# Kernel optimization log

Hardware: AMD Instinct MI355X
Metric: run time of the kernel (lower is better)

The kernel has to match this reference:

```python
import jax, jax.numpy as jnp
import numpy as np
import math

V, D, H, L, F, S, B = 32000, 1024, 16, 4, 4096, 1024, 2
DK = D // H
EPS = 1e-5


def _pe(seq_len, d_model):
    pos = jnp.arange(seq_len, dtype=jnp.float32)[:, None]
    div = jnp.exp(jnp.arange(0, d_model, 2, dtype=jnp.float32) * (-math.log(10000.0) / d_model))
    ang = pos * div  # [S, D/2]
    return jnp.stack([jnp.sin(ang), jnp.cos(ang)], axis=-1).reshape(seq_len, d_model)


def _ln(x, g, b):
    m = jnp.mean(x, axis=-1, keepdims=True)
    v = jnp.mean(jnp.square(x - m), axis=-1, keepdims=True)
    return (x - m) * jax.lax.rsqrt(v + EPS) * g + b


def setup_inputs() -> dict:
    key = jax.random.key(0)
    ks = jax.random.split(key, 12)
    std = 0.02
    inp = {
        "input_ids": jax.random.randint(ks[0], (B, S), 0, V, dtype=jnp.int32),
        "embed": std * jax.random.normal(ks[1], (V, D), dtype=jnp.float32),
        "Wq": std * jax.random.normal(ks[2], (L, D, D), dtype=jnp.float32),
        "bq": jnp.zeros((L, D), jnp.float32),
        "Wk": std * jax.random.normal(ks[3], (L, D, D), dtype=jnp.float32),
        "bk": jnp.zeros((L, D), jnp.float32),
        "Wv": std * jax.random.normal(ks[4], (L, D, D), dtype=jnp.float32),
        "bv": jnp.zeros((L, D), jnp.float32),
        "Wo": std * jax.random.normal(ks[5], (L, D, D), dtype=jnp.float32),
        "bo": jnp.zeros((L, D), jnp.float32),
        "ln1_g": jnp.ones((L, D), jnp.float32), "ln1_b": jnp.zeros((L, D), jnp.float32),
        "W1": std * jax.random.normal(ks[6], (L, F, D), dtype=jnp.float32),
        "b1": jnp.zeros((L, F), jnp.float32),
        "W2": std * jax.random.normal(ks[7], (L, D, F), dtype=jnp.float32),
        "b2": jnp.zeros((L, D), jnp.float32),
        "ln2_g": jnp.ones((L, D), jnp.float32), "ln2_b": jnp.zeros((L, D), jnp.float32),
        "lnf_g": jnp.ones((D,), jnp.float32), "lnf_b": jnp.zeros((D,), jnp.float32),
        "head_w": std * jax.random.normal(ks[8], (V, D), dtype=jnp.float32),
    }
    return inp


def _forward(input_ids, embed, Wq, bq, Wk, bk, Wv, bv, Wo, bo,
             ln1_g, ln1_b, W1, b1, W2, b2, ln2_g, ln2_b, lnf_g, lnf_b, head_w):
    b, s = input_ids.shape
    x = embed[input_ids] * jnp.float32(math.sqrt(D))  # [B,S,D]
    x = x + _pe(s, D)[None, :, :]
    causal = jnp.tril(jnp.ones((s, s), dtype=bool))  # [S,S]
    scale = jnp.float32(1.0 / math.sqrt(DK))
    for l in range(L):
        q = (x @ Wq[l].T + bq[l]).reshape(b, s, H, DK).transpose(0, 2, 1, 3)
        k = (x @ Wk[l].T + bk[l]).reshape(b, s, H, DK).transpose(0, 2, 1, 3)
        v = (x @ Wv[l].T + bv[l]).reshape(b, s, H, DK).transpose(0, 2, 1, 3)
        scores = jnp.einsum('bhqd,bhkd->bhqk', q, k) * scale
        scores = jnp.where(causal[None, None], scores, jnp.float32(-1e9))
        attn = jax.nn.softmax(scores, axis=-1)
        o = jnp.einsum('bhqk,bhkd->bhqd', attn, v).transpose(0, 2, 1, 3).reshape(b, s, D)
        o = o @ Wo[l].T + bo[l]
        x = _ln(x + o, ln1_g[l], ln1_b[l])
        ff = jax.nn.relu(x @ W1[l].T + b1[l]) @ W2[l].T + b2[l]
        x = _ln(x + ff, ln2_g[l], ln2_b[l])
    x = _ln(x, lnf_g, lnf_b)
    return x @ head_w.T  # logits [B,S,V]


def reference(input_ids, embed, Wq, bq, Wk, bk, Wv, bv, Wo, bo,
              ln1_g, ln1_b, W1, b1, W2, b2, ln2_g, ln2_b, lnf_g, lnf_b, head_w):
    return _forward(input_ids, embed, Wq, bq, Wk, bk, Wv, bv, Wo, bo,
                    ln1_g, ln1_b, W1, b1, W2, b2, ln2_g, ln2_b, lnf_g, lnf_b, head_w)
```

## Files before the change

kernel.cpp:

```cpp
#include <hip/hip_runtime.h>
#include <math.h>


namespace {
constexpr int kV  = 32000;
constexpr int kD  = 1024;
constexpr int kH  = 16;
constexpr int kL  = 4;
constexpr int kF  = 4096;
constexpr int kS  = 1024;
constexpr int kB  = 2;
constexpr int kDK = 64;
constexpr int kM  = kB * kS;
constexpr float kEps   = 1e-5f;
constexpr float kScale = 0.125f;
}

using short8 = __attribute__((ext_vector_type(8))) short;
using f32x4  = __attribute__((ext_vector_type(4))) float;

__device__ __forceinline__ unsigned short f2bf(float f) {
  union { float f; unsigned int u; } x{f};
  const unsigned int r = x.u + 0x7fffu + ((x.u >> 16) & 1u);
  return (unsigned short)(r >> 16);
}

__device__ __forceinline__ void llds16(const void* g, void* l) {
  __builtin_amdgcn_global_load_lds(
      (const __attribute__((address_space(1))) unsigned int*)g,
      (__attribute__((address_space(3))) unsigned int*)l, 16, 0, 0);
}

__device__ __forceinline__ float block_sum256(float v, float* scratch) {
#pragma unroll
  for (int off = 32; off > 0; off >>= 1) v += __shfl_down(v, off, 64);
  const int wid  = threadIdx.x >> 6;
  const int lane = threadIdx.x & 63;
  __syncthreads();
  if (lane == 0) scratch[wid] = v;
  __syncthreads();
  return scratch[0] + scratch[1] + scratch[2] + scratch[3];
}

__global__ __launch_bounds__(256) void f2bf_kernel(const float* __restrict__ in,
                                                   unsigned short* __restrict__ out,
                                                   int n4) {
  const int i = blockIdx.x * 256 + threadIdx.x;
  if (i < n4) {
    const float4 v = ((const float4*)in)[i];
    ushort4 o;
    o.x = f2bf(v.x); o.y = f2bf(v.y); o.z = f2bf(v.z); o.w = f2bf(v.w);
    ((ushort4*)out)[i] = o;
  }
}

__global__ __launch_bounds__(256) void f2bf_layer_kernel(
    const float* __restrict__ wq, const float* __restrict__ wk,
    const float* __restrict__ wv, const float* __restrict__ wo,
    const float* __restrict__ w1, const float* __restrict__ w2,
    unsigned short* __restrict__ dst) {
  const int i = blockIdx.x * 256 + threadIdx.x;
  const float* src;
  size_t so, doff;
  if (i < 1048576) {
    const int seg = i >> 18;
    const int off = i & 262143;
    src = (seg == 0) ? wq : (seg == 1) ? wk : (seg == 2) ? wv : wo;
    so = off;
    doff = (size_t)seg * 1048576 + (size_t)off * 4;
  } else {
    const int j = i - 1048576;
    if (j < 1048576) { src = w1; so = j; doff = 4194304 + (size_t)j * 4; }
    else             { src = w2; so = j - 1048576; doff = 8388608 + (size_t)(j - 1048576) * 4; }
  }
  const float4 v = ((const float4*)src)[so];
  ushort4 o;
  o.x = f2bf(v.x); o.y = f2bf(v.y); o.z = f2bf(v.z); o.w = f2bf(v.w);
  *(ushort4*)(dst + doff) = o;
}

__global__ __launch_bounds__(256) void embed_pe_kernel(
    const int* __restrict__ ids, const float* __restrict__ embed,
    float* __restrict__ x, unsigned short* __restrict__ xb) {
  const int row = blockIdx.x;
  const int s   = row & (kS - 1);
  const int id  = ids[row];
  const float* erow = embed + (size_t)id * kD;
#pragma unroll
  for (int i = 0; i < kD / 256; ++i) {
    const int d = threadIdx.x + i * 256;
    const int p = d >> 1;
    const double div = exp((double)(2 * p) * (-9.210340371976184 / 1024.0));
    const double ang = (double)s * div;
    const float pe = (d & 1) ? (float)cos(ang) : (float)sin(ang);
    const float v = erow[d] * 32.0f + pe;
    x[(size_t)row * kD + d]  = v;
    xb[(size_t)row * kD + d] = f2bf(v);
  }
}

template <int MODE>
__device__ __forceinline__ void gemm_core(int bm, int bn,
                                          const unsigned short* __restrict__ A,
                                          const unsigned short* __restrict__ W,
                                          const float* __restrict__ bias,
                                          void* __restrict__ Cout,
                                          int M, int N, int K,
                                          int k0begin, int k0end, float oscale) {
  __shared__ __align__(16) unsigned short As[128 * 32];
  __shared__ __align__(16) unsigned short Ws[128 * 32];
  const int t    = threadIdx.x;
  const int lane = t & 63;
  const int w    = t >> 6;
  const int wm   = (w >> 1) * 64;
  const int wn   = (w & 1) * 64;
  const int l15  = lane & 15;
  const int quad = lane >> 4;

  f32x4 acc[4][4] = {};

  for (int k0 = k0begin; k0 < k0end; k0 += 32) {
    __syncthreads();
#pragma unroll
    for (int i = 0; i < 2; ++i) {
      const int e   = i * 256 + t;
      const int row = e >> 2;
      const int kc  = (e & 3) * 8;
      const int ldsoff = (i * 256 + w * 64) * 8;
      llds16(A + (size_t)(bm + row) * K + k0 + kc, &As[ldsoff]);
      llds16(W + (size_t)(bn + row) * K + k0 + kc, &Ws[ldsoff]);
    }
    __syncthreads();
    short8 af[4], bf[4];
#pragma unroll
    for (int i = 0; i < 4; ++i)
      af[i] = *(const short8*)&As[(wm + i * 16 + l15) * 32 + quad * 8];
#pragma unroll
    for (int j = 0; j < 4; ++j)
      bf[j] = *(const short8*)&Ws[(wn + j * 16 + l15) * 32 + quad * 8];
#pragma unroll
    for (int i = 0; i < 4; ++i)
#pragma unroll
      for (int j = 0; j < 4; ++j)
        acc[i][j] = __builtin_amdgcn_mfma_f32_16x16x32_bf16(af[i], bf[j], acc[i][j], 0, 0, 0);
  }

#pragma unroll
  for (int i = 0; i < 4; ++i) {
#pragma unroll
    for (int r = 0; r < 4; ++r) {
      const int m = bm + wm + i * 16 + quad * 4 + r;
#pragma unroll
      for (int j = 0; j < 4; ++j) {
        const int n = bn + wn + j * 16 + l15;
        float v = acc[i][j][r] + (bias ? bias[n] : 0.0f);
        if (MODE == 2) v = fmaxf(v, 0.0f);
        if (MODE == 0) {
          ((float*)Cout)[(size_t)m * N + n] = v;
        } else if (MODE == 1) {
          const int b = m >> 10, s = m & 1023;
          const int h = n >> 6,  dk = n & 63;
          ((unsigned short*)Cout)[((size_t)(b * kH + h) * kS + s) * kDK + dk] = f2bf(v * oscale);
        } else if (MODE == 3) {
          const int b = m >> 10, s = m & 1023;
          const int h = n >> 6,  dk = n & 63;
          ((unsigned short*)Cout)[((size_t)(b * kH + h) * kDK + dk) * kS + s] = f2bf(v);
        } else {
          ((unsigned short*)Cout)[(size_t)m * N + n] = f2bf(v);
        }
      }
    }
  }
}

__global__ __launch_bounds__(256) void gemm_head_kernel(
    const unsigned short* __restrict__ A, const unsigned short* __restrict__ W,
    float* __restrict__ C) {
  const int bid = blockIdx.x;
  const int wg  = (bid & 7) * 500 + (bid >> 3);
  const int bm  = (wg & 15) * 128;
  const int bn  = (wg >> 4) * 128;
  gemm_core<0>(bm, bn, A, W, nullptr, C, kM, kV, kD, 0, kD, 1.0f);
}

__global__ __launch_bounds__(256) void gemm_qkv_kernel(
    const unsigned short* __restrict__ A,
    const unsigned short* __restrict__ wq, const unsigned short* __restrict__ wk,
    const unsigned short* __restrict__ wv,
    const float* __restrict__ bq_, const float* __restrict__ bk_,
    const float* __restrict__ bv_,
    unsigned short* __restrict__ qo, unsigned short* __restrict__ ko,
    unsigned short* __restrict__ vo) {
  const int bm = blockIdx.y * 128;
  const int bn = blockIdx.x * 128;
  const int z  = blockIdx.z;
  if (z == 0) {
    gemm_core<1>(bm, bn, A, wq, bq_, qo, kM, kD, kD, 0, kD, kScale);
  } else if (z == 1) {
    gemm_core<1>(bm, bn, A, wk, bk_, ko, kM, kD, kD, 0, kD, 1.0f);
  } else {
    gemm_core<3>(bm, bn, A, wv, bv_, vo, kM, kD, kD, 0, kD, 1.0f);
  }
}

__global__ __launch_bounds__(256) void gemm_splitk_kernel(
    const unsigned short* __restrict__ A, const unsigned short* __restrict__ W,
    const float* __restrict__ bias, float* __restrict__ C0,
    float* __restrict__ C1, int M, int N, int K) {
  const int bm = blockIdx.y * 128;
  const int bn = blockIdx.x * 128;
  if (blockIdx.z == 0)
    gemm_core<0>(bm, bn, A, W, bias, C0, M, N, K, 0, K / 2, 1.0f);
  else
    gemm_core<0>(bm, bn, A, W, nullptr, C1, M, N, K, K / 2, K, 1.0f);
}

__global__ __launch_bounds__(256) void gemm_bf16relu_kernel(
    const unsigned short* __restrict__ A, const unsigned short* __restrict__ W,
    const float* __restrict__ bias, unsigned short* __restrict__ C,
    int M, int N, int K) {
  gemm_core<2>(blockIdx.y * 128, blockIdx.x * 128, A, W, bias, C, M, N, K, 0, K, 1.0f);
}

__global__ __launch_bounds__(256) void attn_mfma_kernel(
    const unsigned short* __restrict__ q, const unsigned short* __restrict__ k,
    const unsigned short* __restrict__ vt, unsigned short* __restrict__ ob) {
  const int bid = blockIdx.x;
  const int wg  = (bid & 7) * 64 + (bid >> 3);
  const int qt  = wg & 15;
  const int h   = (wg >> 4) & 15;
  const int b   = wg >> 8;
  const int q0  = qt * 64;

  __shared__ __align__(16) unsigned short Ks[2][64 * 64];
  __shared__ __align__(16) unsigned short Vs[2][64 * 64];
  __shared__ __align__(16) unsigned short Ps[4][16 * 64];

  const int t    = threadIdx.x;
  const int lane = t & 63;
  const int w    = t >> 6;
  const int l15  = lane & 15;
  const int quad = lane >> 4;

  const size_t base = (size_t)(b * kH + h) * kS * kDK;

  auto stage = [&](int kt_, int buf) {
#pragma unroll
    for (int i = 0; i < 2; ++i) {
      const int e   = i * 256 + t;
      const int row = e >> 3;
      const int g   = e & 7;
      llds16(k + base + (size_t)(kt_ * 64 + row) * kDK + ((g ^ (row & 7)) * 8),
             &Ks[buf][(i * 256 + w * 64) * 8]);
      llds16(vt + base + (size_t)row * kS + kt_ * 64 + ((g ^ (row & 7)) * 8),
             &Vs[buf][(i * 256 + w * 64) * 8]);
    }
  };

  short8 aq[2];
#pragma unroll
  for (int ks = 0; ks < 2; ++ks)
    aq[ks] = *(const short8*)(q + base + (size_t)(q0 + w * 16 + l15) * kDK + ks * 32 + quad * 8);

  f32x4 acc_o[4] = {};
  float m[4]    = {-1e30f, -1e30f, -1e30f, -1e30f};
  float lsum[4] = {0.f, 0.f, 0.f, 0.f};

  stage(0, 0);
  __syncthreads();

  for (int kt = 0; kt <= qt; ++kt) {
    const int cur = kt & 1;
    if (kt < qt) stage(kt + 1, cur ^ 1);

    f32x4 s[4] = {};
#pragma unroll
    for (int j = 0; j < 4; ++j) {
#pragma unroll
      for (int ks = 0; ks < 2; ++ks) {
        const short8 bk8 = *(const short8*)&Ks[cur][(j * 16 + l15) * 64 +
                                                   (((ks * 4 + quad) ^ (l15 & 7)) * 8)];
        s[j] = __builtin_amdgcn_mfma_f32_16x16x32_bf16(aq[ks], bk8, s[j], 0, 0, 0);
      }
    }

    if (kt == qt) {
      const int rb = w * 16 + quad * 4;
#pragma unroll
      for (int j = 0; j < 4; ++j) {
        const int kg = j * 16 + l15;
#pragma unroll
        for (int r = 0; r < 4; ++r)
          if (kg > rb + r) s[j][r] = -1e30f;
      }
    }

    float pm[4];
#pragma unroll
    for (int r = 0; r < 4; ++r)
      pm[r] = fmaxf(fmaxf(s[0][r], s[1][r]), fmaxf(s[2][r], s[3][r]));
#pragma unroll
    for (int off = 8; off > 0; off >>= 1)
#pragma unroll
      for (int r = 0; r < 4; ++r)
        pm[r] = fmaxf(pm[r], __shfl_xor(pm[r], off, 64));

    float alpha[4];
#pragma unroll
    for (int r = 0; r < 4; ++r) {
      const float mn = fmaxf(m[r], pm[r]);
      alpha[r] = __expf(m[r] - mn);
      m[r] = mn;
    }

    float rs[4] = {0.f, 0.f, 0.f, 0.f};
    unsigned short pb16[4][4];
#pragma unroll
    for (int j = 0; j < 4; ++j)
#pragma unroll
      for (int r = 0; r < 4; ++r) {
        const float e = __expf(s[j][r] - m[r]);
        rs[r] += e;
        pb16[j][r] = f2bf(e);
      }
#pragma unroll
    for (int off = 8; off > 0; off >>= 1)
#pragma unroll
      for (int r = 0; r < 4; ++r)
        rs[r] += __shfl_xor(rs[r], off, 64);
#pragma unroll
    for (int r = 0; r < 4; ++r) lsum[r] = lsum[r] * alpha[r] + rs[r];
#pragma unroll
    for (int jd = 0; jd < 4; ++jd)
#pragma unroll
      for (int r = 0; r < 4; ++r) acc_o[jd][r] *= alpha[r];

#pragma unroll
    for (int j = 0; j < 4; ++j)
#pragma unroll
      for (int r = 0; r < 4; ++r) {
        const int row = quad * 4 + r;
        const int col = j * 16 + l15;
        Ps[w][row * 64 + (((col >> 3) ^ (row & 7)) << 3) + (col & 7)] = pb16[j][r];
      }
    asm volatile("s_waitcnt lgkmcnt(0)" ::: "memory");
    __builtin_amdgcn_sched_barrier(0);

    short8 ap[2];
#pragma unroll
    for (int ks = 0; ks < 2; ++ks)
      ap[ks] = *(const short8*)&Ps[w][l15 * 64 + (((ks * 4 + quad) ^ (l15 & 7)) * 8)];

#pragma unroll
    for (int jd = 0; jd < 4; ++jd) {
#pragma unroll
      for (int ks = 0; ks < 2; ++ks) {
        const short8 bv8 = *(const short8*)&Vs[cur][(jd * 16 + l15) * 64 +
                                                   (((ks * 4 + quad) ^ (l15 & 7)) * 8)];
        acc_o[jd] = __builtin_amdgcn_mfma_f32_16x16x32_bf16(ap[ks], bv8, acc_o[jd], 0, 0, 0);
      }
    }

    __syncthreads();
  }

  float inv[4];
#pragma unroll
  for (int r = 0; r < 4; ++r) inv[r] = 1.0f / lsum[r];
#pragma unroll
  for (int jd = 0; jd < 4; ++jd)
#pragma unroll
    for (int r = 0; r < 4; ++r) {
      const int qg = q0 + w * 16 + quad * 4 + r;
      ob[(size_t)(b * kS + qg) * kD + h * kDK + jd * 16 + l15] =
          f2bf(acc_o[jd][r] * inv[r]);
    }
}

__global__ __launch_bounds__(256) void add_ln_kernel(
    float* __restrict__ x, const float* __restrict__ res,
    const float* __restrict__ res2,
    const float* __restrict__ g, const float* __restrict__ bta,
    unsigned short* __restrict__ xb) {
  const int row = blockIdx.x;
  const int t   = threadIdx.x;
  __shared__ float scratch[4];
  float vals[4];
  float sum = 0.f;
  float* xrow = x + (size_t)row * kD;
#pragma unroll
  for (int i = 0; i < 4; ++i) {
    const int d = t + i * 256;
    float vv = xrow[d];
    if (res)  vv += res[(size_t)row * kD + d];
    if (res2) vv += res2[(size_t)row * kD + d];
    vals[i] = vv;
    sum += vv;
  }
  const float mean = block_sum256(sum, scratch) * (1.0f / kD);
  float vsum = 0.f;
#pragma unroll
  for (int i = 0; i < 4; ++i) {
    const float dd = vals[i] - mean;
    vsum += dd * dd;
  }
  const float var  = block_sum256(vsum, scratch) * (1.0f / kD);
  const float rstd = rsqrtf(var + kEps);
#pragma unroll
  for (int i = 0; i < 4; ++i) {
    const int d = t + i * 256;
    const float o = (vals[i] - mean) * rstd * g[d] + bta[d];
    xrow[d] = o;
    xb[(size_t)row * kD + d] = f2bf(o);
  }
}

extern "C" void kernel_launch(void* const* d_in, const int* in_sizes, int n_in,
                              void* d_out, int out_size, void* d_ws, size_t ws_size,
                              hipStream_t stream) {
  const int*   ids   = (const int*)  d_in[0];
  const float* embed = (const float*)d_in[1];
  const float* Wq    = (const float*)d_in[2];
  const float* bq    = (const float*)d_in[3];
  const float* Wk    = (const float*)d_in[4];
  const float* bk    = (const float*)d_in[5];
  const float* Wv    = (const float*)d_in[6];
  const float* bv    = (const float*)d_in[7];
  const float* Wo    = (const float*)d_in[8];
  const float* bo    = (const float*)d_in[9];
  const float* ln1g  = (const float*)d_in[10];
  const float* ln1b  = (const float*)d_in[11];
  const float* W1    = (const float*)d_in[12];
  const float* b1    = (const float*)d_in[13];
  const float* W2    = (const float*)d_in[14];
  const float* b2    = (const float*)d_in[15];
  const float* ln2g  = (const float*)d_in[16];
  const float* ln2b  = (const float*)d_in[17];
  const float* lnfg  = (const float*)d_in[18];
  const float* lnfb  = (const float*)d_in[19];
  const float* headw = (const float*)d_in[20];

  char* ws = (char*)d_ws;
  float*          x    = (float*)          (ws);
  unsigned short* xb   = (unsigned short*) (ws + 8388608);
  unsigned short* qbb  = (unsigned short*) (ws + 12582912);
  unsigned short* kbb  = (unsigned short*) (ws + 16777216);
  unsigned short* vtb  = (unsigned short*) (ws + 20971520);
  unsigned short* ob   = (unsigned short*) (ws + 25165824);
  unsigned short* ff1b = (unsigned short*) (ws + 29360128);
  float*          pb   = (float*)          (ws + 46137344);
  float*          pb2  = (float*)          (ws + 54525952);
  unsigned short* wbuf = (unsigned short*) (ws + 67108864);

  const dim3 blk(256);
  embed_pe_kernel<<<kM, blk, 0, stream>>>(ids, embed, x, xb);

  for (int l = 0; l < kL; ++l) {
    const size_t oD = (size_t)l * kD * kD;
    const size_t oF = (size_t)l * kF * kD;
    f2bf_layer_kernel<<<12288, blk, 0, stream>>>(
        Wq + oD, Wk + oD, Wv + oD, Wo + oD, W1 + oF, W2 + oF, wbuf);

    gemm_qkv_kernel<<<dim3(8, 16, 3), blk, 0, stream>>>(
        xb, wbuf, wbuf + 1048576, wbuf + 2097152,
        bq + (size_t)l * kD, bk + (size_t)l * kD, bv + (size_t)l * kD,
        qbb, kbb, vtb);
    attn_mfma_kernel<<<kB * kH * (kS / 64), blk, 0, stream>>>(qbb, kbb, vtb, ob);
    gemm_splitk_kernel<<<dim3(8, 16, 2), blk, 0, stream>>>(
        ob, wbuf + 3145728, bo + (size_t)l * kD, pb, pb2, kM, kD, kD);
    add_ln_kernel<<<kM, blk, 0, stream>>>(
        x, pb, pb2, ln1g + (size_t)l * kD, ln1b + (size_t)l * kD, xb);
    gemm_bf16relu_kernel<<<dim3(32, 16), blk, 0, stream>>>(
        xb, wbuf + 4194304, b1 + (size_t)l * kF, ff1b, kM, kF, kD);
    gemm_splitk_kernel<<<dim3(8, 16, 2), blk, 0, stream>>>(
        ff1b, wbuf + 8388608, b2 + (size_t)l * kD, pb, pb2, kM, kD, kF);
    add_ln_kernel<<<kM, blk, 0, stream>>>(
        x, pb, pb2, ln2g + (size_t)l * kD, ln2b + (size_t)l * kD, xb);
  }

  add_ln_kernel<<<kM, blk, 0, stream>>>(x, nullptr, nullptr, lnfg, lnfb, xb);
  f2bf_kernel<<<32000, blk, 0, stream>>>(headw, wbuf, 8192000);
  gemm_head_kernel<<<dim3(4000), blk, 0, stream>>>(xb, wbuf, (float*)d_out);
}
```

Measured before the change: 1.533 ms.

## Use 256x256-tile, 512-thread, 4-stage pipelined GEMM for LM head

Replaces the generic 128x128 LM-head GEMM with a dedicated 256x256-tile kernel using 8 waves, a 4-deep LDS ring buffer filled by direct-to-LDS loads, and explicit vmcnt waits. Each wave computes a 128x64 sub-tile. Larger tiles raise arithmetic intensity and cut re-reads of A and W, and the deeper prefetch hides global latency. In exchange it uses more registers (128 accumulator floats per lane) and 128KB of LDS, giving lower occupancy and only 1000 blocks for the device.

Result: no change. 1.553 ms (+1.3%).

```diff
diff --git a/kernel.cpp b/kernel.cpp
--- a/kernel.cpp
+++ b/kernel.cpp
@@ -173,14 +173,85 @@
   }
 }
 
-__global__ __launch_bounds__(256) void gemm_head_kernel(
+__global__ __launch_bounds__(512) void gemm_head256_kernel(
     const unsigned short* __restrict__ A, const unsigned short* __restrict__ W,
     float* __restrict__ C) {
   const int bid = blockIdx.x;
-  const int wg  = (bid & 7) * 500 + (bid >> 3);
-  const int bm  = (wg & 15) * 128;
-  const int bn  = (wg >> 4) * 128;
-  gemm_core<0>(bm, bn, A, W, nullptr, C, kM, kV, kD, 0, kD, 1.0f);
+  const int wg  = (bid & 7) * 125 + (bid >> 3);
+  const int bm  = (wg & 7) * 256;
+  const int bn  = (wg >> 3) * 256;
+
+  __shared__ __align__(16) unsigned short As[4][256 * 32];
+  __shared__ __align__(16) unsigned short Bs[4][256 * 32];
+
+  const int t    = threadIdx.x;
+  const int lane = t & 63;
+  const int w    = t >> 6;
+  const int wm   = (w >> 2) * 128;
+  const int wn   = (w & 3) * 64;
+  const int l15  = lane & 15;
+  const int quad = lane >> 4;
+  constexpr int NT = kD / 32;
+
+  auto stage = [&](int kt, int buf) {
+#pragma unroll
+    for (int i = 0; i < 2; ++i) {
+      const int e   = i * 512 + t;
+      const int row = e >> 2;
+      const int g   = e & 3;
+      const int ldsoff = (i * 512 + w * 64) * 8;
+      llds16(A + (size_t)(bm + row) * kD + kt * 32 + ((g ^ (row & 3)) * 8),
+             &As[buf][ldsoff]);
+      llds16(W + (size_t)(bn + row) * kD + kt * 32 + ((g ^ (row & 3)) * 8),
+             &Bs[buf][ldsoff]);
+    }
+  };
+
+  f32x4 acc[8][4] = {};
+
+  stage(0, 0); stage(1, 1); stage(2, 2);
+
+  for (int kt = 0; kt < NT; ++kt) {
+    const int buf = kt & 3;
+    if (kt + 3 < NT) stage(kt + 3, (kt + 3) & 3);
+    if (kt <= NT - 4)      asm volatile("s_waitcnt vmcnt(12)" ::: "memory");
+    else if (kt == NT - 3) asm volatile("s_waitcnt vmcnt(8)"  ::: "memory");
+    else if (kt == NT - 2) asm volatile("s_waitcnt vmcnt(4)"  ::: "memory");
+    else                   asm volatile("s_waitcnt vmcnt(0)"  ::: "memory");
+    __builtin_amdgcn_s_barrier();
+    asm volatile("" ::: "memory");
+
+    short8 bf[4];
+#pragma unroll
+    for (int j = 0; j < 4; ++j) {
+      const int rb = wn + j * 16 + l15;
+      bf[j] = *(const short8*)&Bs[buf][rb * 32 + ((quad ^ (rb & 3)) * 8)];
+    }
+    __builtin_amdgcn_s_setprio(1);
+#pragma unroll
+    for (int i = 0; i < 8; ++i) {
+      const int ra = wm + i * 16 + l15;
+      const short8 af = *(const short8*)&As[buf][ra * 32 + ((quad ^ (ra & 3)) * 8)];
+#pragma unroll
+      for (int j = 0; j < 4; ++j)
+        acc[i][j] = __builtin_amdgcn_mfma_f32_16x16x32_bf16(af, bf[j], acc[i][j], 0, 0, 0);
+    }
+    __builtin_amdgcn_s_setprio(0);
+    asm volatile("" ::: "memory");
+    __builtin_amdgcn_s_barrier();
+  }
+
+#pragma unroll
+  for (int i = 0; i < 8; ++i)
+#pragma unroll
+    for (int r = 0; r < 4; ++r) {
+      const int m = bm + wm + i * 16 + quad * 4 + r;
+#pragma unroll
+      for (int j = 0; j < 4; ++j) {
+        const int n = bn + wn + j * 16 + l15;
+        C[(size_t)m * kV + n] = acc[i][j][r];
+      }
+    }
 }
 
 __global__ __launch_bounds__(256) void gemm_qkv_kernel(
@@ -480,5 +551,5 @@
 
   add_ln_kernel<<<kM, blk, 0, stream>>>(x, nullptr, nullptr, lnfg, lnfb, xb);
   f2bf_kernel<<<32000, blk, 0, stream>>>(headw, wbuf, 8192000);
-  gemm_head_kernel<<<dim3(4000), blk, 0, stream>>>(xb, wbuf, (float*)d_out);
-}
+  gemm_head256_kernel<<<dim3(1000), dim3(512), 0, stream>>>(xb, wbuf, (float*)d_out);
+}
```
